# Optimization experiments

Measured on AMD Instinct MI355X. Metric: run time of the kernel, lower is better.

The kernel has to match this reference:

```python
import jax, jax.numpy as jnp
import numpy as np
import math

B, N, H = 32, 512, 512  # batch, nodes_num (=input_dim), hidden_dim; upscale=1.0 -> d_qk = H


def setup_inputs() -> dict:
    key = jax.random.key(0)
    ks = jax.random.split(key, 4)
    s = 1.0 / math.sqrt(H)
    x = jax.random.normal(ks[0], (B, N, H), dtype=jnp.float32)
    Wq = jax.random.normal(ks[1], (H, H), dtype=jnp.float32) * s
    Wk = jax.random.normal(ks[2], (H, H), dtype=jnp.float32) * s
    Wm = jax.random.normal(ks[3], (N * H, H), dtype=jnp.float32) * (1.0 / math.sqrt(N * H))
    return {
        "x": x,
        "Wq": Wq, "bq": jnp.zeros((H,), jnp.float32),
        "Wk": Wk, "bk": jnp.zeros((H,), jnp.float32),
        "Wm": Wm, "bm": jnp.zeros((H,), jnp.float32),
    }


def reference(x, Wq, bq, Wk, bk, Wm, bm):
    # q/k projections (Linear stored as (in, out))
    q = jnp.einsum('bnh,hd->bnd', x, Wq) + bq          # [B,N,D]
    k = jnp.einsum('bnh,hd->bnd', x, Wk) + bk          # [B,N,D]
    d = q.shape[-1]
    scores = jnp.einsum('bnd,bmd->bnm', q, k) / math.sqrt(d)
    attention = jax.nn.softmax(jax.nn.sigmoid(scores), axis=-1)  # [B,N,N]
    out = jnp.einsum('bnm,bmh->bnh', attention, x)     # dropout = identity (eval)
    b, n, h = x.shape
    out = out.reshape(b, n * h) @ Wm + bm              # [B,H]
    return (out, attention)
```

## Files before the change

### kernel.cpp

```cpp
#include <hip/hip_runtime.h>

#define BB 32
#define NN 512
#define HH 512
constexpr float QK_SCALE = 0.04419417382415922f;

using bf16x8 = __attribute__((ext_vector_type(8))) short;
using f32x4  = __attribute__((ext_vector_type(4))) float;

__device__ __forceinline__ short f2bf(float f) {
  unsigned int u = __float_as_uint(f);
  unsigned int r = (u + 0x7FFFu + ((u >> 16) & 1u)) >> 16;
  return (short)r;
}

__global__ __launch_bounds__(256) void prep_x(const float* __restrict__ x,
                                              short* __restrict__ xbf,
                                              short* __restrict__ xT) {
  __shared__ float tile[32][33];
  const int b = blockIdx.z;
  const int n0 = blockIdx.y * 32, h0 = blockIdx.x * 32;
  const int t = threadIdx.x;
  const int i = t >> 3;
  const int j4 = (t & 7) * 4;
  const float4 v = *(const float4*)&x[((long)b * NN + n0 + i) * HH + h0 + j4];
  short o[4] = {f2bf(v.x), f2bf(v.y), f2bf(v.z), f2bf(v.w)};
  *(uint2*)&xbf[((long)b * NN + n0 + i) * HH + h0 + j4] = *(uint2*)o;
  tile[i][j4 + 0] = v.x; tile[i][j4 + 1] = v.y;
  tile[i][j4 + 2] = v.z; tile[i][j4 + 3] = v.w;
  __syncthreads();
  short p[4] = {f2bf(tile[j4 + 0][i]), f2bf(tile[j4 + 1][i]),
                f2bf(tile[j4 + 2][i]), f2bf(tile[j4 + 3][i])};
  *(uint2*)&xT[((long)b * HH + h0 + i) * NN + n0 + j4] = *(uint2*)p;
}

__global__ __launch_bounds__(256) void prep_w(const float* __restrict__ Wq,
                                              const float* __restrict__ Wk,
                                              short* __restrict__ Wqt,
                                              short* __restrict__ Wkt) {
  __shared__ float tile[32][33];
  const float* W = blockIdx.z ? Wk : Wq;
  short* Wt = blockIdx.z ? Wkt : Wqt;
  const int h0 = blockIdx.y * 32, d0 = blockIdx.x * 32;
  const int t = threadIdx.x;
  const int i = t >> 3;
  const int j4 = (t & 7) * 4;
  const float4 v = *(const float4*)&W[(long)(h0 + i) * HH + d0 + j4];
  tile[i][j4 + 0] = v.x; tile[i][j4 + 1] = v.y;
  tile[i][j4 + 2] = v.z; tile[i][j4 + 3] = v.w;
  __syncthreads();
  short p[4] = {f2bf(tile[j4 + 0][i]), f2bf(tile[j4 + 1][i]),
                f2bf(tile[j4 + 2][i]), f2bf(tile[j4 + 3][i])};
  *(uint2*)&Wt[(long)(d0 + i) * HH + h0 + j4] = *(uint2*)p;
}

template <int WRITE_BF16>
__global__ __launch_bounds__(256) void gemm_bt(const short* __restrict__ A,
                                               const short* __restrict__ Bt,
                                               void* __restrict__ Cv,
                                               const float* __restrict__ bias,
                                               float scale, int M, int Nc, int K,
                                               long sA, long sB, long sC) {
  __shared__ short As[64][72];
  __shared__ short Bs[64][72];
  A += (long)blockIdx.z * sA;
  Bt += (long)blockIdx.z * sB;
  const int m0 = blockIdx.x * 64;
  const int n0 = blockIdx.y * 64;
  const int t = threadIdx.x;
  const int wave = t >> 6, lane = t & 63;
  const int lrow = lane & 15, lq = lane >> 4;
  const int srow = t >> 2;
  const int scol = (t & 3) * 16;
  f32x4 acc[4] = {};
  const short* Ar = A + (long)(m0 + srow) * K + scol;
  const short* Br = Bt + (long)(n0 + srow) * K + scol;
  for (int k0 = 0; k0 < K; k0 += 64) {
    *(uint4*)&As[srow][scol]     = *(const uint4*)&Ar[k0];
    *(uint4*)&As[srow][scol + 8] = *(const uint4*)&Ar[k0 + 8];
    *(uint4*)&Bs[srow][scol]     = *(const uint4*)&Br[k0];
    *(uint4*)&Bs[srow][scol + 8] = *(const uint4*)&Br[k0 + 8];
    __syncthreads();
#pragma unroll
    for (int kk = 0; kk < 64; kk += 32) {
      bf16x8 a = *(bf16x8*)&As[wave * 16 + lrow][kk + lq * 8];
#pragma unroll
      for (int nt = 0; nt < 4; ++nt) {
        bf16x8 b = *(bf16x8*)&Bs[nt * 16 + lrow][kk + lq * 8];
        acc[nt] = __builtin_amdgcn_mfma_f32_16x16x32_bf16(a, b, acc[nt], 0, 0, 0);
      }
    }
    __syncthreads();
  }
  const long cbase = (long)blockIdx.z * sC;
#pragma unroll
  for (int nt = 0; nt < 4; ++nt) {
#pragma unroll
    for (int r = 0; r < 4; ++r) {
      const int row = m0 + wave * 16 + lq * 4 + r;
      const int col = n0 + nt * 16 + lrow;
      float v = acc[nt][r] * scale;
      if (bias) v += bias[col];
      if (WRITE_BF16)
        ((short*)Cv)[cbase + (long)row * Nc + col] = f2bf(v);
      else
        ((float*)Cv)[cbase + (long)row * Nc + col] = v;
    }
  }
}

__global__ __launch_bounds__(256) void sigsoftmax(float* __restrict__ att,
                                                  short* __restrict__ attbf) {
  const long row = blockIdx.x;
  float* p = att + row * NN;
  const int t = threadIdx.x;
  float2 v = *(float2*)&p[t * 2];
  const float s0 = 1.f / (1.f + __expf(-v.x));
  const float s1 = 1.f / (1.f + __expf(-v.y));
  const float e0 = __expf(s0), e1 = __expf(s1);
  float sum = e0 + e1;
#pragma unroll
  for (int o = 32; o > 0; o >>= 1) sum += __shfl_down(sum, o);
  __shared__ float wsum[4];
  if ((t & 63) == 0) wsum[t >> 6] = sum;
  __syncthreads();
  const float r = 1.f / (wsum[0] + wsum[1] + wsum[2] + wsum[3]);
  const float a0 = e0 * r, a1 = e1 * r;
  float2 o2; o2.x = a0; o2.y = a1;
  *(float2*)&p[t * 2] = o2;
  short pk[2] = {f2bf(a0), f2bf(a1)};
  *(unsigned int*)&attbf[row * NN + t * 2] = *(unsigned int*)pk;
}

__global__ __launch_bounds__(256) void init_out(float* __restrict__ out,
                                                const float* __restrict__ bm) {
  const int t = blockIdx.x * 256 + threadIdx.x;
  out[t] = bm[t & (HH - 1)];
}

__global__ __launch_bounds__(256) void gemm_final(const short* __restrict__ A,
                                                  const float* __restrict__ Wm,
                                                  float* __restrict__ out) {
  __shared__ short As[32][40];
  __shared__ short Bs[64][40];
  const int j0 = blockIdx.y * 64;
  const long KT = (long)NN * HH;
  const long Kc = KT / gridDim.x;
  const long i0base = (long)blockIdx.x * Kc;
  const int t = threadIdx.x;
  const int wave = t >> 6, lane = t & 63;
  const int lrow = lane & 15, lq = lane >> 4;
  const int jj = t & 63;
  const int rb = (t >> 6) * 8;
  f32x4 acc[2] = {};
  for (long i0 = i0base; i0 < i0base + Kc; i0 += 32) {
    if (t < 128) {
      const int ar = t >> 2;
      const int ac = (t & 3) * 8;
      *(uint4*)&As[ar][ac] = *(const uint4*)&A[(long)ar * KT + i0 + ac];
    }
#pragma unroll
    for (int r = 0; r < 8; ++r) {
      Bs[jj][rb + r] = f2bf(Wm[(i0 + rb + r) * HH + j0 + jj]);
    }
    __syncthreads();
    bf16x8 b  = *(bf16x8*)&Bs[wave * 16 + lrow][lq * 8];
    bf16x8 a0 = *(bf16x8*)&As[lrow][lq * 8];
    bf16x8 a1 = *(bf16x8*)&As[16 + lrow][lq * 8];
    acc[0] = __builtin_amdgcn_mfma_f32_16x16x32_bf16(a0, b, acc[0], 0, 0, 0);
    acc[1] = __builtin_amdgcn_mfma_f32_16x16x32_bf16(a1, b, acc[1], 0, 0, 0);
    __syncthreads();
  }
#pragma unroll
  for (int mt = 0; mt < 2; ++mt)
#pragma unroll
    for (int r = 0; r < 4; ++r) {
      const int brow = mt * 16 + lq * 4 + r;
      const int col = j0 + wave * 16 + lrow;
      atomicAdd(&out[(long)brow * HH + col], acc[mt][r]);
    }
}

extern "C" void kernel_launch(void* const* d_in, const int* in_sizes, int n_in,
                              void* d_out, int out_size, void* d_ws, size_t ws_size,
                              hipStream_t stream) {
  const float* x  = (const float*)d_in[0];
  const float* Wq = (const float*)d_in[1];
  const float* bq = (const float*)d_in[2];
  const float* Wk = (const float*)d_in[3];
  const float* bk = (const float*)d_in[4];
  const float* Wm = (const float*)d_in[5];
  const float* bm = (const float*)d_in[6];
  float* out = (float*)d_out;
  float* att = out + (long)BB * HH;

  char* ws = (char*)d_ws;
  const long SZ = (long)BB * NN * HH * sizeof(short);
  short* buf0 = (short*)ws;
  short* buf1 = (short*)(ws + SZ);
  short* buf2 = (short*)(ws + 2 * SZ);
  short* buf3 = (short*)(ws + 3 * SZ);
  short* wqt  = (short*)(ws + 4 * SZ);
  short* wkt  = wqt + (long)HH * HH;

  prep_x<<<dim3(HH / 32, NN / 32, BB), 256, 0, stream>>>(x, buf0, buf1);
  prep_w<<<dim3(HH / 32, HH / 32, 2), 256, 0, stream>>>(Wq, Wk, wqt, wkt);

  gemm_bt<1><<<dim3(BB * NN / 64, HH / 64, 1), 256, 0, stream>>>(
      buf0, wqt, buf2, bq, 1.f, BB * NN, HH, HH, 0, 0, 0);
  gemm_bt<1><<<dim3(BB * NN / 64, HH / 64, 1), 256, 0, stream>>>(
      buf0, wkt, buf3, bk, 1.f, BB * NN, HH, HH, 0, 0, 0);

  gemm_bt<0><<<dim3(NN / 64, NN / 64, BB), 256, 0, stream>>>(
      buf2, buf3, att, nullptr, QK_SCALE, NN, NN, HH,
      (long)NN * HH, (long)NN * HH, (long)NN * NN);

  sigsoftmax<<<dim3(BB * NN), 256, 0, stream>>>(att, buf2);

  gemm_bt<1><<<dim3(NN / 64, HH / 64, BB), 256, 0, stream>>>(
      buf2, buf1, buf0, nullptr, 1.f, NN, HH, NN,
      (long)NN * NN, (long)HH * NN, (long)NN * HH);

  init_out<<<dim3(BB * HH / 256), 256, 0, stream>>>(out, bm);
  gemm_final<<<dim3(256, HH / 64, 1), 256, 0, stream>>>(buf0, Wm, out);
}
```

Measured before the change: 833.8 us.

## Use 128x128 GEMM tiles with direct-to-LDS loads and fp32 split-K final projection

Replaces the 64x64 GEMM with a 128x128 tile kernel that uses global_load_lds for staging and a 4x4 MFMA register block per wave. The Q and K projections are merged into one launch via the z dimension. The attention-times-x output is now kept in fp32. The final Wm projection is rewritten as an fp32 FMA split-K pass that writes partial sums, followed by a separate reduce kernel, which replaces the atomic-based bf16 MFMA version. This aims to raise data reuse in the big GEMMs and to read Wm once without per-element conversion and atomics. In exchange it adds fp32 traffic for the intermediate buffer and the partials, and the final stage moves from matrix cores to scalar FMA.

```diff
diff --git a/kernel.cpp b/kernel.cpp
--- a/kernel.cpp
+++ b/kernel.cpp
@@ -3,6 +3,7 @@
 #define BB 32
 #define NN 512
 #define HH 512
+#define KT (NN * HH)
 constexpr float QK_SCALE = 0.04419417382415922f;
 
 using bf16x8 = __attribute__((ext_vector_type(8))) short;
@@ -13,6 +14,11 @@
   unsigned int r = (u + 0x7FFFu + ((u >> 16) & 1u)) >> 16;
   return (short)r;
 }
+
+#define GLOAD_LDS16(g, l)                                              \
+  __builtin_amdgcn_global_load_lds(                                    \
+      (const __attribute__((address_space(1))) void*)(g),              \
+      (__attribute__((address_space(3))) void*)(l), 16, 0, 0)
 
 __global__ __launch_bounds__(256) void prep_x(const float* __restrict__ x,
                                               short* __restrict__ xbf,
@@ -55,58 +61,70 @@
 }
 
 template <int WRITE_BF16>
-__global__ __launch_bounds__(256) void gemm_bt(const short* __restrict__ A,
+__global__ __launch_bounds__(256) void gemm128(const short* __restrict__ A,
                                                const short* __restrict__ Bt,
                                                void* __restrict__ Cv,
-                                               const float* __restrict__ bias,
-                                               float scale, int M, int Nc, int K,
+                                               const float* __restrict__ bias0,
+                                               const float* __restrict__ bias1,
+                                               float scale, int Nc, int K,
                                                long sA, long sB, long sC) {
-  __shared__ short As[64][72];
-  __shared__ short Bs[64][72];
-  A += (long)blockIdx.z * sA;
-  Bt += (long)blockIdx.z * sB;
-  const int m0 = blockIdx.x * 64;
-  const int n0 = blockIdx.y * 64;
-  const int t = threadIdx.x;
-  const int wave = t >> 6, lane = t & 63;
+  __shared__ short As[128 * 64];
+  __shared__ short Bs[128 * 64];
+  const int z = blockIdx.z;
+  A += (long)z * sA;
+  Bt += (long)z * sB;
+  const float* bias = (z & 1) ? bias1 : bias0;
+  const int m0 = blockIdx.x * 128, n0 = blockIdx.y * 128;
+  const int t = threadIdx.x, wave = t >> 6, lane = t & 63;
   const int lrow = lane & 15, lq = lane >> 4;
-  const int srow = t >> 2;
-  const int scol = (t & 3) * 16;
-  f32x4 acc[4] = {};
-  const short* Ar = A + (long)(m0 + srow) * K + scol;
-  const short* Br = Bt + (long)(n0 + srow) * K + scol;
+  const int wm = wave & 1, wn = wave >> 1;
+  const int sgrow = lane >> 3;
+  const int sgcol = (lane & 7) * 8;
+  f32x4 acc[4][4] = {};
   for (int k0 = 0; k0 < K; k0 += 64) {
-    *(uint4*)&As[srow][scol]     = *(const uint4*)&Ar[k0];
-    *(uint4*)&As[srow][scol + 8] = *(const uint4*)&Ar[k0 + 8];
-    *(uint4*)&Bs[srow][scol]     = *(const uint4*)&Br[k0];
-    *(uint4*)&Bs[srow][scol + 8] = *(const uint4*)&Br[k0 + 8];
+#pragma unroll
+    for (int r = 0; r < 4; ++r) {
+      const int s = wave * 4 + r;
+      const short* ga = A + (long)(m0 + s * 8 + sgrow) * K + k0 + sgcol;
+      const short* gb = Bt + (long)(n0 + s * 8 + sgrow) * K + k0 + sgcol;
+      GLOAD_LDS16(ga, As + s * 512);
+      GLOAD_LDS16(gb, Bs + s * 512);
+    }
     __syncthreads();
 #pragma unroll
     for (int kk = 0; kk < 64; kk += 32) {
-      bf16x8 a = *(bf16x8*)&As[wave * 16 + lrow][kk + lq * 8];
-#pragma unroll
-      for (int nt = 0; nt < 4; ++nt) {
-        bf16x8 b = *(bf16x8*)&Bs[nt * 16 + lrow][kk + lq * 8];
-        acc[nt] = __builtin_amdgcn_mfma_f32_16x16x32_bf16(a, b, acc[nt], 0, 0, 0);
-      }
+      bf16x8 af[4], bf[4];
+#pragma unroll
+      for (int mt = 0; mt < 4; ++mt)
+        af[mt] = *(const bf16x8*)&As[(wm * 64 + mt * 16 + lrow) * 64 + kk + lq * 8];
+#pragma unroll
+      for (int nt = 0; nt < 4; ++nt)
+        bf[nt] = *(const bf16x8*)&Bs[(wn * 64 + nt * 16 + lrow) * 64 + kk + lq * 8];
+#pragma unroll
+      for (int mt = 0; mt < 4; ++mt)
+#pragma unroll
+        for (int nt = 0; nt < 4; ++nt)
+          acc[mt][nt] = __builtin_amdgcn_mfma_f32_16x16x32_bf16(
+              af[mt], bf[nt], acc[mt][nt], 0, 0, 0);
     }
     __syncthreads();
   }
-  const long cbase = (long)blockIdx.z * sC;
-#pragma unroll
-  for (int nt = 0; nt < 4; ++nt) {
-#pragma unroll
-    for (int r = 0; r < 4; ++r) {
-      const int row = m0 + wave * 16 + lq * 4 + r;
-      const int col = n0 + nt * 16 + lrow;
-      float v = acc[nt][r] * scale;
-      if (bias) v += bias[col];
-      if (WRITE_BF16)
-        ((short*)Cv)[cbase + (long)row * Nc + col] = f2bf(v);
-      else
-        ((float*)Cv)[cbase + (long)row * Nc + col] = v;
-    }
-  }
+  const long cb = (long)z * sC;
+#pragma unroll
+  for (int mt = 0; mt < 4; ++mt)
+#pragma unroll
+    for (int nt = 0; nt < 4; ++nt)
+#pragma unroll
+      for (int r = 0; r < 4; ++r) {
+        const int row = m0 + wm * 64 + mt * 16 + lq * 4 + r;
+        const int col = n0 + wn * 64 + nt * 16 + lrow;
+        float v = acc[mt][nt][r] * scale;
+        if (bias) v += bias[col];
+        if (WRITE_BF16)
+          ((short*)Cv)[cb + (long)row * Nc + col] = f2bf(v);
+        else
+          ((float*)Cv)[cb + (long)row * Nc + col] = v;
+      }
 }
 
 __global__ __launch_bounds__(256) void sigsoftmax(float* __restrict__ att,
@@ -132,53 +150,42 @@
   *(unsigned int*)&attbf[row * NN + t * 2] = *(unsigned int*)pk;
 }
 
-__global__ __launch_bounds__(256) void init_out(float* __restrict__ out,
-                                                const float* __restrict__ bm) {
-  const int t = blockIdx.x * 256 + threadIdx.x;
-  out[t] = bm[t & (HH - 1)];
-}
-
-__global__ __launch_bounds__(256) void gemm_final(const short* __restrict__ A,
-                                                  const float* __restrict__ Wm,
-                                                  float* __restrict__ out) {
-  __shared__ short As[32][40];
-  __shared__ short Bs[64][40];
-  const int j0 = blockIdx.y * 64;
-  const long KT = (long)NN * HH;
-  const long Kc = KT / gridDim.x;
-  const long i0base = (long)blockIdx.x * Kc;
-  const int t = threadIdx.x;
-  const int wave = t >> 6, lane = t & 63;
-  const int lrow = lane & 15, lq = lane >> 4;
-  const int jj = t & 63;
-  const int rb = (t >> 6) * 8;
-  f32x4 acc[2] = {};
-  for (long i0 = i0base; i0 < i0base + Kc; i0 += 32) {
-    if (t < 128) {
-      const int ar = t >> 2;
-      const int ac = (t & 3) * 8;
-      *(uint4*)&As[ar][ac] = *(const uint4*)&A[(long)ar * KT + i0 + ac];
+__global__ __launch_bounds__(256) void final_partial(const float* __restrict__ out1,
+                                                     const float* __restrict__ Wm,
+                                                     float* __restrict__ part) {
+  const int j = blockIdx.y * 256 + threadIdx.x;
+  const long kc = KT / gridDim.x;
+  const long k0 = (long)blockIdx.x * kc;
+  float acc[BB] = {};
+  for (long k = k0; k < k0 + kc; k += 8) {
+    float w[8];
+#pragma unroll
+    for (int kk = 0; kk < 8; ++kk) w[kk] = Wm[(k + kk) * HH + j];
+#pragma unroll
+    for (int b = 0; b < BB; ++b) {
+#pragma unroll
+      for (int kk = 0; kk < 8; ++kk)
+        acc[b] = fmaf(out1[(long)b * KT + k + kk], w[kk], acc[b]);
     }
-#pragma unroll
-    for (int r = 0; r < 8; ++r) {
-      Bs[jj][rb + r] = f2bf(Wm[(i0 + rb + r) * HH + j0 + jj]);
-    }
-    __syncthreads();
-    bf16x8 b  = *(bf16x8*)&Bs[wave * 16 + lrow][lq * 8];
-    bf16x8 a0 = *(bf16x8*)&As[lrow][lq * 8];
-    bf16x8 a1 = *(bf16x8*)&As[16 + lrow][lq * 8];
-    acc[0] = __builtin_amdgcn_mfma_f32_16x16x32_bf16(a0, b, acc[0], 0, 0, 0);
-    acc[1] = __builtin_amdgcn_mfma_f32_16x16x32_bf16(a1, b, acc[1], 0, 0, 0);
-    __syncthreads();
   }
-#pragma unroll
-  for (int mt = 0; mt < 2; ++mt)
-#pragma unroll
-    for (int r = 0; r < 4; ++r) {
-      const int brow = mt * 16 + lq * 4 + r;
-      const int col = j0 + wave * 16 + lrow;
-      atomicAdd(&out[(long)brow * HH + col], acc[mt][r]);
-    }
+  float* p = part + (long)blockIdx.x * (BB * HH);
+#pragma unroll
+  for (int b = 0; b < BB; ++b) p[(long)b * HH + j] = acc[b];
+}
+
+__global__ __launch_bounds__(256) void final_reduce(const float* __restrict__ part,
+                                                    const float* __restrict__ bm,
+                                                    float* __restrict__ out, int S) {
+  __shared__ float red[4][64];
+  const int fi = blockIdx.x * 64 + (threadIdx.x & 63);
+  const int sg = threadIdx.x >> 6;
+  float s = 0.f;
+  for (int i = sg; i < S; i += 4) s += part[(long)i * (BB * HH) + fi];
+  red[sg][threadIdx.x & 63] = s;
+  __syncthreads();
+  if (sg == 0)
+    out[fi] = bm[fi & (HH - 1)] + red[0][threadIdx.x] + red[1][threadIdx.x] +
+              red[2][threadIdx.x] + red[3][threadIdx.x];
 }
 
 extern "C" void kernel_launch(void* const* d_in, const int* in_sizes, int n_in,
@@ -195,32 +202,32 @@
   float* att = out + (long)BB * HH;
 
   char* ws = (char*)d_ws;
-  const long SZ = (long)BB * NN * HH * sizeof(short);
-  short* buf0 = (short*)ws;
-  short* buf1 = (short*)(ws + SZ);
-  short* buf2 = (short*)(ws + 2 * SZ);
-  short* buf3 = (short*)(ws + 3 * SZ);
-  short* wqt  = (short*)(ws + 4 * SZ);
-  short* wkt  = wqt + (long)HH * HH;
-
-  prep_x<<<dim3(HH / 32, NN / 32, BB), 256, 0, stream>>>(x, buf0, buf1);
+  const long SZ = (long)BB * NN * HH * 2;
+  short* xbf   = (short*)ws;
+  short* xT    = (short*)(ws + SZ);
+  short* qb    = (short*)(ws + 2 * SZ);
+  short* kb    = (short*)(ws + 3 * SZ);
+  short* wqt   = (short*)(ws + 4 * SZ);
+  short* wkt   = wqt + (long)HH * HH;
+  float* out1f = (float*)(ws + 4 * SZ + 4 * (long)HH * HH);
+  float* part  = out1f + (long)BB * KT;
+
+  prep_x<<<dim3(HH / 32, NN / 32, BB), 256, 0, stream>>>(x, xbf, xT);
   prep_w<<<dim3(HH / 32, HH / 32, 2), 256, 0, stream>>>(Wq, Wk, wqt, wkt);
 
-  gemm_bt<1><<<dim3(BB * NN / 64, HH / 64, 1), 256, 0, stream>>>(
-      buf0, wqt, buf2, bq, 1.f, BB * NN, HH, HH, 0, 0, 0);
-  gemm_bt<1><<<dim3(BB * NN / 64, HH / 64, 1), 256, 0, stream>>>(
-      buf0, wkt, buf3, bk, 1.f, BB * NN, HH, HH, 0, 0, 0);
-
-  gemm_bt<0><<<dim3(NN / 64, NN / 64, BB), 256, 0, stream>>>(
-      buf2, buf3, att, nullptr, QK_SCALE, NN, NN, HH,
+  gemm128<1><<<dim3(BB * NN / 128, HH / 128, 2), 256, 0, stream>>>(
+      xbf, wqt, qb, bq, bk, 1.f, HH, HH, 0, (long)HH * HH, (long)BB * NN * HH);
+
+  gemm128<0><<<dim3(NN / 128, NN / 128, BB), 256, 0, stream>>>(
+      qb, kb, att, nullptr, nullptr, QK_SCALE, NN, HH,
       (long)NN * HH, (long)NN * HH, (long)NN * NN);
 
-  sigsoftmax<<<dim3(BB * NN), 256, 0, stream>>>(att, buf2);
-
-  gemm_bt<1><<<dim3(NN / 64, HH / 64, BB), 256, 0, stream>>>(
-      buf2, buf1, buf0, nullptr, 1.f, NN, HH, NN,
+  sigsoftmax<<<dim3(BB * NN), 256, 0, stream>>>(att, qb);
+
+  gemm128<0><<<dim3(NN / 128, HH / 128, BB), 256, 0, stream>>>(
+      qb, xT, out1f, nullptr, nullptr, 1.f, HH, NN,
       (long)NN * NN, (long)HH * NN, (long)NN * HH);
 
-  init_out<<<dim3(BB * HH / 256), 256, 0, stream>>>(out, bm);
-  gemm_final<<<dim3(256, HH / 64, 1), 256, 0, stream>>>(buf0, Wm, out);
-}
+  final_partial<<<dim3(512, 2), 256, 0, stream>>>(out1f, Wm, part);
+  final_reduce<<<dim3(BB * HH / 64), 256, 0, stream>>>(part, bm, out, 512);
+}
```

Measured after the change: 1.568 ms. 1.88x slower.
